# Optimization experiments

Measured on AMD Instinct MI355X. Metric: run time of the kernel, lower is better.

The kernel has to match this reference:

```python
import jax, jax.numpy as jnp
import numpy as np

N, S, E, H = 4, 2048, 1024, 16
D = E // H  # head dim = 64


def setup_inputs() -> dict:
    key = jax.random.key(0)
    ks = jax.random.split(key, 8)
    return {
        "values": jax.random.normal(ks[0], (N, S, E), dtype=jnp.float32),
        "keys": jax.random.normal(ks[1], (N, S, E), dtype=jnp.float32),
        "queries": jax.random.normal(ks[2], (N, S, E), dtype=jnp.float32),
        "mask": jnp.ones((N, 1, 1, S), dtype=jnp.int32),
        "Wv": jax.random.normal(ks[3], (D, D), dtype=jnp.float32) / np.sqrt(D),
        "Wk": jax.random.normal(ks[4], (D, D), dtype=jnp.float32) / np.sqrt(D),
        "Wq": jax.random.normal(ks[5], (D, D), dtype=jnp.float32) / np.sqrt(D),
        "W_out": jax.random.normal(ks[6], (E, E), dtype=jnp.float32) / np.sqrt(E),
        "b_out": jnp.zeros((E,), dtype=jnp.float32),
    }


def reference(values, keys, queries, mask, Wv, Wk, Wq, W_out, b_out):
    n, q_len = queries.shape[0], queries.shape[1]
    v = values.reshape(n, -1, H, D)
    k = keys.reshape(n, -1, H, D)
    q = queries.reshape(n, q_len, H, D)
    # per-head linear projections (torch Linear: x @ W.T), shared across heads
    v = jnp.einsum('nlhd,ed->nlhe', v, Wv)
    k = jnp.einsum('nlhd,ed->nlhe', k, Wk)
    q = jnp.einsum('nqhd,ed->nqhe', q, Wq)
    # full score tensor [n, h, q, k], faithful to the original einsum
    energy = jnp.einsum('nqhd,nkhd->nhqk', q, k)
    energy = jnp.where(mask == 0, jnp.float32(-1e20), energy)
    # NOTE: original scales by sqrt(embed_size), not sqrt(head_dim)
    attention = jax.nn.softmax(energy / jnp.sqrt(jnp.float32(E)), axis=3)
    out = jnp.einsum('nhql,nlhd->nqhd', attention, v).reshape(n, q_len, E)
    out = out @ W_out.T + b_out
    return out
```

## Files before the change

### kernel.cpp

```cpp
#include <hip/hip_runtime.h>
#include <stdint.h>

#define N_B 4
#define SEQ 2048
#define EMB 1024
#define NH  16
#define HD  64
#define NHT 64
#define BQ  256
#define BK  64

typedef __attribute__((ext_vector_type(8))) short bf16x8;
typedef __attribute__((ext_vector_type(4))) float f32x4;
typedef __attribute__((ext_vector_type(2))) unsigned int u32x2;

__device__ __forceinline__ short f2bf(float x) {
  unsigned u = __float_as_uint(x);
  u += 0x7fffu + ((u >> 16) & 1u);
  return (short)(u >> 16);
}

#if __has_builtin(__builtin_amdgcn_cvt_pk_bf16_f32)
typedef __attribute__((ext_vector_type(2))) __bf16 bf16v2;
__device__ __forceinline__ unsigned pkbf(float a, float b) {
  bf16v2 r = __builtin_amdgcn_cvt_pk_bf16_f32(a, b);
  union { bf16v2 v; unsigned u; } c; c.v = r; return c.u;
}
#else
__device__ __forceinline__ unsigned pkbf(float a, float b) {
  return (unsigned)(unsigned short)f2bf(a) | ((unsigned)(unsigned short)f2bf(b) << 16);
}
#endif

__device__ __forceinline__ void swap32p(unsigned a, unsigned b, unsigned& r0, unsigned& r1) {
#if __has_builtin(__builtin_amdgcn_permlane32_swap)
  u32x2 r = __builtin_amdgcn_permlane32_swap(a, b, false, false);
  r0 = r[0]; r1 = r[1];
#else
  unsigned as = (unsigned)__shfl_xor((int)a, 32, 64), bs = (unsigned)__shfl_xor((int)b, 32, 64);
  int lo = (threadIdx.x & 32) == 0;
  r0 = lo ? a : bs;
  r1 = lo ? as : b;
#endif
}
__device__ __forceinline__ void swap16p(unsigned a, unsigned b, unsigned& r0, unsigned& r1) {
#if __has_builtin(__builtin_amdgcn_permlane16_swap)
  u32x2 r = __builtin_amdgcn_permlane16_swap(a, b, false, false);
  r0 = r[0]; r1 = r[1];
#else
  unsigned as = (unsigned)__shfl_xor((int)a, 16, 64), bs = (unsigned)__shfl_xor((int)b, 16, 64);
  int ev = (threadIdx.x & 16) == 0;
  r0 = ev ? a : bs;
  r1 = ev ? as : b;
#endif
}

__device__ __forceinline__ void glds16(const short* g, short* l) {
  __builtin_amdgcn_global_load_lds(
      (const __attribute__((address_space(1))) unsigned int*)g,
      (__attribute__((address_space(3))) unsigned int*)l, 16, 0, 0);
}

__device__ __forceinline__ int swz_src(int lane) {
  return (((lane & 7) ^ ((lane >> 3) & 7)) * 8) + ((lane >> 3) * 64);
}
__device__ __forceinline__ int swz_rd(int r, int k) {
  return r * 64 + ((k ^ (r & 7)) * 8);
}

__global__ __launch_bounds__(256) void projm_kernel(
    const float* __restrict__ Xq, const float* __restrict__ Xk, const float* __restrict__ Xv,
    const float* __restrict__ Wq, const float* __restrict__ Wk, const float* __restrict__ Wv,
    short* __restrict__ Qp, short* __restrict__ Kp, short* __restrict__ Vp,
    const float* __restrict__ Wo, short* __restrict__ Wb) {
  int tid = threadIdx.x;
  int z = blockIdx.z;
  if (z == 3) {
    int flat = blockIdx.x + blockIdx.y * 16;
    int idx = (flat * 256 + tid) * 4;
    f32x4 v = *(const f32x4*)(Wo + idx);
    uint2 u; u.x = pkbf(v.x, v.y); u.y = pkbf(v.z, v.w);
    *(uint2*)(Wb + idx) = u;
    return;
  }
  const float* X = (z == 0) ? Xq : (z == 1) ? Xk : Xv;
  const float* W = (z == 0) ? Wq : (z == 1) ? Wk : Wv;
  short* out = (z == 0) ? Qp : (z == 1) ? Kp : Vp;
  int transposed = (z == 2);
  float oscale = (z == 0) ? 0.04508422f : 1.0f;

  __shared__ __attribute__((aligned(16))) short Xs[128 * 64];
  __shared__ __attribute__((aligned(16))) short Ws[64 * 64];
  int w = tid >> 6, lane = tid & 63;
  int quad = lane >> 4, l15 = lane & 15;
  int sb = blockIdx.x * 128;
  int nh = blockIdx.y;
  int n = nh >> 4, h = nh & 15;
  int r4 = tid >> 2, c0 = (tid & 3) * 16;
  int ch0 = c0 >> 3;
#pragma unroll
  for (int rr = 0; rr < 2; rr++) {
    int row = rr * 64 + r4;
    const float* gp = X + ((size_t)(n * SEQ + sb + row)) * EMB + h * HD + c0;
    f32x4 a = *(const f32x4*)gp, b = *(const f32x4*)(gp + 4);
    f32x4 c = *(const f32x4*)(gp + 8), d = *(const f32x4*)(gp + 12);
    uint4 u0, u1;
    u0.x = pkbf(a.x, a.y); u0.y = pkbf(a.z, a.w);
    u0.z = pkbf(b.x, b.y); u0.w = pkbf(b.z, b.w);
    u1.x = pkbf(c.x, c.y); u1.y = pkbf(c.z, c.w);
    u1.z = pkbf(d.x, d.y); u1.w = pkbf(d.z, d.w);
    *(uint4*)&Xs[row * 64 + ((ch0 ^ (row & 7)) * 8)] = u0;
    *(uint4*)&Xs[row * 64 + (((ch0 + 1) ^ (row & 7)) * 8)] = u1;
  }
  {
    int e = r4;
    const float* wp = W + e * HD + c0;
    f32x4 a = *(const f32x4*)wp, b = *(const f32x4*)(wp + 4);
    f32x4 c = *(const f32x4*)(wp + 8), d = *(const f32x4*)(wp + 12);
    uint4 u0, u1;
    u0.x = pkbf(a.x, a.y); u0.y = pkbf(a.z, a.w);
    u0.z = pkbf(b.x, b.y); u0.w = pkbf(b.z, b.w);
    u1.x = pkbf(c.x, c.y); u1.y = pkbf(c.z, c.w);
    u1.z = pkbf(d.x, d.y); u1.w = pkbf(d.z, d.w);
    *(uint4*)&Ws[e * 64 + ((ch0 ^ (e & 7)) * 8)] = u0;
    *(uint4*)&Ws[e * 64 + (((ch0 + 1) ^ (e & 7)) * 8)] = u1;
  }
  __syncthreads();
  f32x4 acc[2][4] = {};
#pragma unroll
  for (int ch = 0; ch < 2; ch++) {
    bf16x8 af[2], bfr[4];
#pragma unroll
    for (int mi = 0; mi < 2; mi++)
      af[mi] = *(const bf16x8*)&Xs[swz_rd(w * 32 + mi * 16 + l15, ch * 4 + quad)];
#pragma unroll
    for (int ni = 0; ni < 4; ni++)
      bfr[ni] = *(const bf16x8*)&Ws[swz_rd(ni * 16 + l15, ch * 4 + quad)];
#pragma unroll
    for (int mi = 0; mi < 2; mi++)
#pragma unroll
      for (int ni = 0; ni < 4; ni++)
        acc[mi][ni] = __builtin_amdgcn_mfma_f32_16x16x32_bf16(af[mi], bfr[ni], acc[mi][ni], 0, 0, 0);
  }
  if (!transposed) {
#pragma unroll
    for (int mi = 0; mi < 2; mi++)
#pragma unroll
      for (int ni = 0; ni < 4; ni++)
#pragma unroll
        for (int r = 0; r < 4; r++) {
          int s = sb + w * 32 + mi * 16 + quad * 4 + r;
          out[((size_t)nh * SEQ + s) * HD + ni * 16 + l15] = f2bf(acc[mi][ni][r] * oscale);
        }
  } else {
#pragma unroll
    for (int mi = 0; mi < 2; mi++)
#pragma unroll
      for (int ni = 0; ni < 4; ni++) {
        int e2 = ni * 16 + l15;
        int s0 = sb + w * 32 + mi * 16 + quad * 4;
        uint2 u;
        u.x = pkbf(acc[mi][ni][0], acc[mi][ni][1]);
        u.y = pkbf(acc[mi][ni][2], acc[mi][ni][3]);
        *(uint2*)(out + ((size_t)nh * HD + e2) * SEQ + s0) = u;
      }
  }
}

__global__ __launch_bounds__(512, 4) void attn_kernel(
    const short* __restrict__ Qg, const short* __restrict__ Kg,
    const short* __restrict__ Vg, const int* __restrict__ maskp,
    short* __restrict__ AO) {
  __shared__ __attribute__((aligned(16))) short L[32768];

  int tid = threadIdx.x;
  int w = tid >> 6, lane = tid & 63;
  int quad = lane >> 4, l15 = lane & 15;
  int nh = blockIdx.x;
  int qt0 = blockIdx.y * BQ;
  int n = nh >> 4, h = nh & 15;
  int ssrc = swz_src(lane);
  int vrow = lane >> 3;
  int vcg = (((lane & 7) ^ ((lane >> 3) & 7)) * 8);
  const int NS = SEQ / (2 * BK);

  const short* kb = Kg + (size_t)nh * SEQ * HD;
  const short* vb = Vg + (size_t)nh * HD * SEQ;

  bf16x8 qf[2][2];
  {
    const short* qb = Qg + ((size_t)nh * SEQ + qt0 + w * 32) * HD;
#pragma unroll
    for (int nt = 0; nt < 2; nt++)
#pragma unroll
      for (int ch = 0; ch < 2; ch++)
        qf[nt][ch] = *(const bf16x8*)(qb + (nt * 16 + l15) * HD + ch * 32 + quad * 8);
  }

  auto stage_tile = [&](int t, int base) {
    glds16(kb + (size_t)t * (BK * HD) + w * 512 + ssrc, &L[base + w * 512]);
    int d = w * 8 + vrow;
    glds16(vb + (size_t)d * SEQ + t * BK + vcg, &L[base + 4096 + w * 512]);
  };

  stage_tile(0, 0);
  stage_tile(1, 8192);
  int mA = maskp[n * SEQ + lane];
  int mB = maskp[n * SEQ + BK + lane];
  __syncthreads();

  bf16x8 vone;
#pragma unroll
  for (int j = 0; j < 8; j++) vone[j] = (short)0x3F80;

  f32x4 Oacc[2][4] = {};
  f32x4 lacc[2] = {};

  for (int s = 0; s < NS; s++) {
    int p = s & 1;
    if (s + 1 < NS) {
      int t0 = 2 * s + 2;
      stage_tile(t0, (p ^ 1) * 16384);
      stage_tile(t0 + 1, (p ^ 1) * 16384 + 8192);
    }
    int tn = (s + 1 < NS) ? (2 * s + 2) : 0;
    int mAn = maskp[n * SEQ + tn * BK + lane];
    int mBn = maskp[n * SEQ + (tn + 1) * BK + lane];

#pragma unroll
    for (int j = 0; j < 2; j++) {
      const short* Kb = &L[p * 16384 + j * 8192];
      const short* Vb = Kb + 4096;
      unsigned long long mb = __ballot((j == 0 ? mA : mB) != 0);
      bool anymask = (mb != ~0ull);

#pragma unroll
      for (int half = 0; half < 2; half++) {
        f32x4 st[2][2];
        __builtin_amdgcn_s_setprio(1);
#pragma unroll
        for (int m2 = 0; m2 < 2; m2++) {
          int mt = half * 2 + m2;
          bf16x8 kf0 = *(const bf16x8*)&Kb[swz_rd(mt * 16 + l15, quad)];
          bf16x8 kf1 = *(const bf16x8*)&Kb[swz_rd(mt * 16 + l15, 4 + quad)];
#pragma unroll
          for (int nt = 0; nt < 2; nt++) {
            f32x4 a = {0.f, 0.f, 0.f, 0.f};
            a = __builtin_amdgcn_mfma_f32_16x16x32_bf16(kf0, qf[nt][0], a, 0, 0, 0);
            a = __builtin_amdgcn_mfma_f32_16x16x32_bf16(kf1, qf[nt][1], a, 0, 0, 0);
            st[m2][nt] = a;
          }
        }
        __builtin_amdgcn_s_setprio(0);
        if (anymask) {
#pragma unroll
          for (int m2 = 0; m2 < 2; m2++)
#pragma unroll
            for (int r = 0; r < 4; r++) {
              int kk = (half * 2 + m2) * 16 + quad * 4 + r;
              if (!((mb >> kk) & 1)) { st[m2][0][r] = -1e20f; st[m2][1][r] = -1e20f; }
            }
        }
        bf16x8 pf[2];
#pragma unroll
        for (int nt = 0; nt < 2; nt++) {
          unsigned A0 = pkbf(__builtin_amdgcn_exp2f(st[0][nt][0]), __builtin_amdgcn_exp2f(st[0][nt][1]));
          unsigned A1 = pkbf(__builtin_amdgcn_exp2f(st[0][nt][2]), __builtin_amdgcn_exp2f(st[0][nt][3]));
          unsigned B0 = pkbf(__builtin_amdgcn_exp2f(st[1][nt][0]), __builtin_amdgcn_exp2f(st[1][nt][1]));
          unsigned B1 = pkbf(__builtin_amdgcn_exp2f(st[1][nt][2]), __builtin_amdgcn_exp2f(st[1][nt][3]));
          unsigned r0, r1, s0, s1, o0, o1, o2, o3;
          swap32p(A0, B0, r0, r1);
          swap16p(r0, r1, o0, o2);
          swap32p(A1, B1, s0, s1);
          swap16p(s0, s1, o1, o3);
          union { unsigned u[4]; bf16x8 v; } c;
          c.u[0] = o0; c.u[1] = o1; c.u[2] = o2; c.u[3] = o3;
          pf[nt] = c.v;
        }

        __builtin_amdgcn_s_setprio(1);
#pragma unroll
        for (int qt = 0; qt < 2; qt++)
          lacc[qt] = __builtin_amdgcn_mfma_f32_16x16x32_bf16(pf[qt], vone, lacc[qt], 0, 0, 0);
#pragma unroll
        for (int dt = 0; dt < 4; dt++) {
          bf16x8 vf = *(const bf16x8*)&Vb[swz_rd(dt * 16 + l15, half * 4 + quad)];
#pragma unroll
          for (int qt = 0; qt < 2; qt++)
            Oacc[qt][dt] = __builtin_amdgcn_mfma_f32_16x16x32_bf16(pf[qt], vf, Oacc[qt][dt], 0, 0, 0);
        }
        __builtin_amdgcn_s_setprio(0);
      }
    }
    mA = mAn;
    mB = mBn;
    __syncthreads();
  }
#pragma unroll
  for (int qt = 0; qt < 2; qt++)
#pragma unroll
    for (int r = 0; r < 4; r++) {
      float inv = 1.0f / lacc[qt][r];
      int qrow = qt0 + w * 32 + qt * 16 + quad * 4 + r;
      size_t rowb = ((size_t)n * SEQ + qrow) * EMB + h * HD;
#pragma unroll
      for (int dt = 0; dt < 4; dt++)
        AO[rowb + dt * 16 + l15] = f2bf(Oacc[qt][dt][r] * inv);
    }
}

__global__ __launch_bounds__(256, 2) void gemm_kernel(const short* __restrict__ A,
                                                      const short* __restrict__ B,
                                                      const float* __restrict__ bias,
                                                      float* __restrict__ C) {
  __shared__ __attribute__((aligned(16))) short As[2][128 * 64];
  __shared__ __attribute__((aligned(16))) short Bs[2][128 * 64];
  int tid = threadIdx.x;
  int w = tid >> 6, lane = tid & 63;
  int quad = lane >> 4, l15 = lane & 15;
  int m0 = blockIdx.x * 128, n0 = blockIdx.y * 128;
  int mw = (w & 1) * 64, nw = (w >> 1) * 64;
  int lrow = lane >> 3;
  int lcg = ((lane & 7) ^ ((lane >> 3) & 7)) * 8;
  f32x4 acc[4][4] = {};
#pragma unroll
  for (int i = 0; i < 4; i++) {
    int ii = w * 4 + i;
    int r = ii * 8 + lrow;
    glds16(A + (size_t)(m0 + r) * 1024 + lcg, &As[0][ii * 512]);
    glds16(B + (size_t)(n0 + r) * 1024 + lcg, &Bs[0][ii * 512]);
  }
  __syncthreads();
  for (int kt = 0; kt < 16; kt++) {
    int cur = kt & 1;
    if (kt < 15) {
      int k0n = (kt + 1) * 64;
#pragma unroll
      for (int i = 0; i < 4; i++) {
        int ii = w * 4 + i;
        int r = ii * 8 + lrow;
        glds16(A + (size_t)(m0 + r) * 1024 + k0n + lcg, &As[cur ^ 1][ii * 512]);
        glds16(B + (size_t)(n0 + r) * 1024 + k0n + lcg, &Bs[cur ^ 1][ii * 512]);
      }
    }
#pragma unroll
    for (int ch = 0; ch < 2; ch++) {
      bf16x8 af[4], bfr[4];
#pragma unroll
      for (int mi = 0; mi < 4; mi++)
        af[mi] = *(const bf16x8*)&As[cur][swz_rd(mw + mi * 16 + l15, ch * 4 + quad)];
#pragma unroll
      for (int ni = 0; ni < 4; ni++)
        bfr[ni] = *(const bf16x8*)&Bs[cur][swz_rd(nw + ni * 16 + l15, ch * 4 + quad)];
#pragma unroll
      for (int mi = 0; mi < 4; mi++)
#pragma unroll
        for (int ni = 0; ni < 4; ni++)
          acc[mi][ni] = __builtin_amdgcn_mfma_f32_16x16x32_bf16(af[mi], bfr[ni], acc[mi][ni], 0, 0, 0);
    }
    __syncthreads();
  }
#pragma unroll
  for (int ni = 0; ni < 4; ni++) {
    int col = n0 + nw + ni * 16 + l15;
    float bv = bias[col];
#pragma unroll
    for (int mi = 0; mi < 4; mi++) {
      int rb = m0 + mw + mi * 16 + quad * 4;
#pragma unroll
      for (int r = 0; r < 4; r++)
        C[(size_t)(rb + r) * 1024 + col] = acc[mi][ni][r] + bv;
    }
  }
}

extern "C" void kernel_launch(void* const* d_in, const int* in_sizes, int n_in,
                              void* d_out, int out_size, void* d_ws, size_t ws_size,
                              hipStream_t stream) {
  const float* values  = (const float*)d_in[0];
  const float* keys    = (const float*)d_in[1];
  const float* queries = (const float*)d_in[2];
  const int*   mask    = (const int*)d_in[3];
  const float* Wv = (const float*)d_in[4];
  const float* Wk = (const float*)d_in[5];
  const float* Wq = (const float*)d_in[6];
  const float* Wo = (const float*)d_in[7];
  const float* bo = (const float*)d_in[8];
  float* out = (float*)d_out;

  short* ws = (short*)d_ws;
  short* Qp = ws;
  short* Kp = Qp + (size_t)NHT * SEQ * HD;
  short* Vp = Kp + (size_t)NHT * SEQ * HD;
  short* AO = Vp + (size_t)NHT * SEQ * HD;
  short* Wb = AO + (size_t)N_B * SEQ * EMB;

  dim3 pg(SEQ / 128, NHT, 4);
  projm_kernel<<<pg, dim3(256), 0, stream>>>(queries, keys, values, Wq, Wk, Wv,
                                             Qp, Kp, Vp, Wo, Wb);
  dim3 ag(NHT, SEQ / BQ);
  attn_kernel<<<ag, dim3(512), 0, stream>>>(Qp, Kp, Vp, mask, AO);
  dim3 gg(8192 / 128, 1024 / 128);
  gemm_kernel<<<gg, dim3(256), 0, stream>>>(AO, Wb, bo, out);
}
```

Baseline: 267.7 us.

## Stage projection outputs through LDS for coalesced stores; use 512-thread output GEMM

The projection kernel now writes its bf16 results into shared memory first, then copies them out with 16-byte coalesced global stores. The transposed K output uses an XOR-swizzled layout so those writes no longer turn into scattered 2-byte or 8-byte strided stores. Separately, the output GEMM goes from 256 to 512 threads with 8 waves, each computing a 64x32 sub-tile. Each wave issues half as many loads and holds a smaller accumulator, trading some LDS fragment reuse for higher occupancy and latency hiding. The change adds extra barriers and relies on the Xs buffer being large enough for the staged tile.

```diff
diff --git a/kernel.cpp b/kernel.cpp
--- a/kernel.cpp
+++ b/kernel.cpp
@@ -142,6 +142,7 @@
       for (int ni = 0; ni < 4; ni++)
         acc[mi][ni] = __builtin_amdgcn_mfma_f32_16x16x32_bf16(af[mi], bfr[ni], acc[mi][ni], 0, 0, 0);
   }
+  __syncthreads();
   if (!transposed) {
 #pragma unroll
     for (int mi = 0; mi < 2; mi++)
@@ -149,21 +150,37 @@
       for (int ni = 0; ni < 4; ni++)
 #pragma unroll
         for (int r = 0; r < 4; r++) {
-          int s = sb + w * 32 + mi * 16 + quad * 4 + r;
-          out[((size_t)nh * SEQ + s) * HD + ni * 16 + l15] = f2bf(acc[mi][ni][r] * oscale);
+          int sl = w * 32 + mi * 16 + quad * 4 + r;
+          Xs[sl * 64 + ni * 16 + l15] = f2bf(acc[mi][ni][r] * oscale);
         }
+    __syncthreads();
+    short* gbase = out + ((size_t)nh * SEQ + sb) * HD;
+#pragma unroll
+    for (int rep = 0; rep < 4; rep++) {
+      int g = rep * 256 + tid;
+      *(uint4*)(gbase + g * 8) = *(const uint4*)&Xs[g * 8];
+    }
   } else {
 #pragma unroll
     for (int mi = 0; mi < 2; mi++)
 #pragma unroll
       for (int ni = 0; ni < 4; ni++) {
-        int e2 = ni * 16 + l15;
-        int s0 = sb + w * 32 + mi * 16 + quad * 4;
+        int e = ni * 16 + l15;
+        int sl0 = w * 32 + mi * 16 + quad * 4;
         uint2 u;
         u.x = pkbf(acc[mi][ni][0], acc[mi][ni][1]);
         u.y = pkbf(acc[mi][ni][2], acc[mi][ni][3]);
-        *(uint2*)(out + ((size_t)nh * HD + e2) * SEQ + s0) = u;
+        int chunk = sl0 >> 3, off = sl0 & 7;
+        *(uint2*)&Xs[e * 128 + ((chunk ^ (e & 7)) * 8) + off] = u;
       }
+    __syncthreads();
+#pragma unroll
+    for (int rep = 0; rep < 4; rep++) {
+      int g = rep * 256 + tid;
+      int e = g >> 4, sc = g & 15;
+      *(uint4*)(out + ((size_t)nh * HD + e) * SEQ + sb + sc * 8) =
+          *(const uint4*)&Xs[e * 128 + ((sc ^ (e & 7)) * 8)];
+    }
   }
 }
 
@@ -309,7 +326,7 @@
     }
 }
 
-__global__ __launch_bounds__(256, 2) void gemm_kernel(const short* __restrict__ A,
+__global__ __launch_bounds__(512, 4) void gemm_kernel(const short* __restrict__ A,
                                                       const short* __restrict__ B,
                                                       const float* __restrict__ bias,
                                                       float* __restrict__ C) {
@@ -319,13 +336,14 @@
   int w = tid >> 6, lane = tid & 63;
   int quad = lane >> 4, l15 = lane & 15;
   int m0 = blockIdx.x * 128, n0 = blockIdx.y * 128;
-  int mw = (w & 1) * 64, nw = (w >> 1) * 64;
+  int wr = w >> 2, wc = w & 3;
+  int mw = wr * 64, nw = wc * 32;
   int lrow = lane >> 3;
   int lcg = ((lane & 7) ^ ((lane >> 3) & 7)) * 8;
-  f32x4 acc[4][4] = {};
-#pragma unroll
-  for (int i = 0; i < 4; i++) {
-    int ii = w * 4 + i;
+  f32x4 acc[4][2] = {};
+#pragma unroll
+  for (int i = 0; i < 2; i++) {
+    int ii = w * 2 + i;
     int r = ii * 8 + lrow;
     glds16(A + (size_t)(m0 + r) * 1024 + lcg, &As[0][ii * 512]);
     glds16(B + (size_t)(n0 + r) * 1024 + lcg, &Bs[0][ii * 512]);
@@ -336,8 +354,8 @@
     if (kt < 15) {
       int k0n = (kt + 1) * 64;
 #pragma unroll
-      for (int i = 0; i < 4; i++) {
-        int ii = w * 4 + i;
+      for (int i = 0; i < 2; i++) {
+        int ii = w * 2 + i;
         int r = ii * 8 + lrow;
         glds16(A + (size_t)(m0 + r) * 1024 + k0n + lcg, &As[cur ^ 1][ii * 512]);
         glds16(B + (size_t)(n0 + r) * 1024 + k0n + lcg, &Bs[cur ^ 1][ii * 512]);
@@ -345,23 +363,23 @@
     }
 #pragma unroll
     for (int ch = 0; ch < 2; ch++) {
-      bf16x8 af[4], bfr[4];
+      bf16x8 af[4], bfr[2];
 #pragma unroll
       for (int mi = 0; mi < 4; mi++)
         af[mi] = *(const bf16x8*)&As[cur][swz_rd(mw + mi * 16 + l15, ch * 4 + quad)];
 #pragma unroll
-      for (int ni = 0; ni < 4; ni++)
+      for (int ni = 0; ni < 2; ni++)
         bfr[ni] = *(const bf16x8*)&Bs[cur][swz_rd(nw + ni * 16 + l15, ch * 4 + quad)];
 #pragma unroll
       for (int mi = 0; mi < 4; mi++)
 #pragma unroll
-        for (int ni = 0; ni < 4; ni++)
+        for (int ni = 0; ni < 2; ni++)
           acc[mi][ni] = __builtin_amdgcn_mfma_f32_16x16x32_bf16(af[mi], bfr[ni], acc[mi][ni], 0, 0, 0);
     }
     __syncthreads();
   }
 #pragma unroll
-  for (int ni = 0; ni < 4; ni++) {
+  for (int ni = 0; ni < 2; ni++) {
     int col = n0 + nw + ni * 16 + l15;
     float bv = bias[col];
 #pragma unroll
@@ -401,5 +419,5 @@
   dim3 ag(NHT, SEQ / BQ);
   attn_kernel<<<ag, dim3(512), 0, stream>>>(Qp, Kp, Vp, mask, AO);
   dim3 gg(8192 / 128, 1024 / 128);
-  gemm_kernel<<<gg, dim3(256), 0, stream>>>(AO, Wb, bo, out);
-}
+  gemm_kernel<<<gg, dim3(512), 0, stream>>>(AO, Wb, bo, out);
+}
```

Result: no change. 266.5 us (-0.4%).
